# Performance work log

Measured on AMD Instinct MI355X. Metric: run time of the kernel, lower is better.

The kernel has to match this reference:

```python
import jax, jax.numpy as jnp
import numpy as np

NEAR_ZERO = 1e-6


def hat(w):
    # [..., 3] -> [..., 3, 3] skew-symmetric
    x, y, z = w[..., 0], w[..., 1], w[..., 2]
    O = jnp.zeros_like(x)
    return jnp.stack([jnp.stack([O, -z, y], -1),
                      jnp.stack([z, O, -x], -1),
                      jnp.stack([-y, x, O], -1)], -2)


def matrix_exp6(V):
    # V: [..., 6] twist (w, v) -> [..., 4, 4] SE(3) exp, with near-zero branch as in the torch code
    w, v = V[..., :3], V[..., 3:]
    theta = jnp.linalg.norm(w, axis=-1, keepdims=True)  # [..., 1]
    near = theta < NEAR_ZERO
    safe = jnp.where(near, 1.0, theta)
    Wh = hat(w / safe)
    Wh2 = Wh @ Wh
    t = theta[..., None]  # [..., 1, 1]
    I3 = jnp.eye(3, dtype=V.dtype)
    R = I3 + jnp.sin(t) * Wh + (1.0 - jnp.cos(t)) * Wh2
    R = jnp.where(near[..., None], I3, R)
    G = t * I3 + (1.0 - jnp.cos(t)) * Wh + (t - jnp.sin(t)) * Wh2
    p = jnp.einsum('...ij,...j->...i', G, v / safe)
    p = jnp.where(near, v, p)
    top = jnp.concatenate([R, p[..., None]], -1)
    bot = jnp.broadcast_to(jnp.array([0.0, 0.0, 0.0, 1.0], V.dtype), top.shape[:-2] + (1, 4))
    return jnp.concatenate([top, bot], -2)


def trans_inv(T):
    R = T[..., :3, :3]
    p = T[..., :3, 3]
    Rt = jnp.swapaxes(R, -1, -2)
    pinv = -jnp.einsum('...ij,...j->...i', Rt, p)
    top = jnp.concatenate([Rt, pinv[..., None]], -1)
    bot = jnp.broadcast_to(jnp.array([0.0, 0.0, 0.0, 1.0], T.dtype), top.shape[:-2] + (1, 4))
    return jnp.concatenate([top, bot], -2)


def adjoint(T):
    R = T[..., :3, :3]
    p = T[..., :3, 3]
    Z = jnp.zeros_like(R)
    top = jnp.concatenate([R, Z], -1)
    bot = jnp.concatenate([hat(p) @ R, R], -1)
    return jnp.concatenate([top, bot], -2)


def ad(V):
    W = hat(V[..., :3])
    Vh = hat(V[..., 3:])
    Z = jnp.zeros_like(W)
    top = jnp.concatenate([W, Z], -1)
    bot = jnp.concatenate([Vh, W], -1)
    return jnp.concatenate([top, bot], -2)


def inverse_dynamics(q, dq, ddq, g, Ftip, Alist, Mlist, Glist):
    # q, dq, ddq: [B, JN]; g: [3]; Ftip: [B, 6]; Alist: [JN, 6]; Mlist: [JN+1, 4, 4]; Glist: [JN, 6, 6]
    B, JN = q.shape
    Minv = trans_inv(Mlist)  # [JN+1, 4, 4]
    v0 = jnp.zeros((B, 6), q.dtype)
    a0 = jnp.concatenate([jnp.zeros((B, 3), q.dtype), jnp.broadcast_to(-g, (B, 3))], -1)

    # forward recursion over joints (sequential -> lax.scan), vectorized over batch
    def fwd_step(carry, xs):
        v, a = carry
        A_i, Minv_i, q_i, dq_i, ddq_i = xs
        T = matrix_exp6(-A_i[None, :] * q_i[:, None]) @ Minv_i  # [B, 4, 4]
        Ad = adjoint(T)
        v_new = jnp.einsum('bij,bj->bi', Ad, v) + A_i * dq_i[:, None]
        a_new = (jnp.einsum('bij,bj->bi', Ad, a)
                 + jnp.einsum('bij,j->bi', ad(v_new), A_i) * dq_i[:, None]
                 + A_i * ddq_i[:, None])
        return (v_new, a_new), (T, v_new, a_new)

    _, (Ts, vs, as_) = jax.lax.scan(fwd_step, (v0, a0), (Alist, Minv[:-1], q.T, dq.T, ddq.T))
    T_last = jnp.broadcast_to(Minv[-1], (B, 4, 4))
    AdNext = adjoint(jnp.concatenate([Ts[1:], T_last[None]], 0))  # [JN, B, 6, 6]

    # backward force recursion
    def bwd_step(F, xs):
        AdN, G_i, A_i, v_i, a_i = xs
        F_new = (jnp.einsum('bji,bj->bi', AdN, F)
                 + jnp.einsum('ij,bj->bi', G_i, a_i)
                 - jnp.einsum('bji,jk,bk->bi', ad(v_i), G_i, v_i))
        return F_new, F_new @ A_i

    _, tau = jax.lax.scan(bwd_step, Ftip, (AdNext, Glist, Alist, vs, as_), reverse=True)
    return tau.T  # [B, JN]


def setup_inputs() -> dict:
    key = jax.random.key(0)
    k = jax.random.split(key, 8)
    B, JN = 131072, 9
    q = jax.random.normal(k[0], (B, JN), jnp.float32)
    dq = jax.random.normal(k[1], (B, JN), jnp.float32)
    ddq = jax.random.normal(k[2], (B, JN), jnp.float32)
    Ftip = jax.random.normal(k[3], (B, 6), jnp.float32)
    g = jnp.array([0.0, 0.0, -9.8], jnp.float32)
    # screw axes with unit rotational part (revolute joints)
    w = jax.random.normal(k[4], (JN, 3), jnp.float32)
    w = w / jnp.linalg.norm(w, axis=-1, keepdims=True)
    vlin = jax.random.normal(k[5], (JN, 3), jnp.float32)
    Alist = jnp.concatenate([w, vlin], -1)
    # valid SE(3) home transforms
    Mlist = matrix_exp6(0.5 * jax.random.normal(k[6], (JN + 1, 6), jnp.float32))
    # SPD spatial inertias
    S = 0.3 * jax.random.normal(k[7], (JN, 6, 6), jnp.float32)
    Glist = S @ jnp.swapaxes(S, -1, -2) + jnp.eye(6, dtype=jnp.float32)
    return {"q": q, "dq": dq, "ddq": ddq, "g": g, "Ftip": Ftip,
            "Alist": Alist, "Mlist": Mlist, "Glist": Glist}


def reference(q, dq, ddq, g, Ftip, Alist, Mlist, Glist):
    return inverse_dynamics(q, dq, ddq, g, Ftip, Alist, Mlist, Glist)
```

## Files before the change

### kernel.cpp

```cpp
#include <hip/hip_runtime.h>
#include <math.h>

#define JN 9
#define BLK 128

__device__ __forceinline__ void mat3_vec(const float* R, const float* x, float* y) {
    y[0] = R[0]*x[0] + R[1]*x[1] + R[2]*x[2];
    y[1] = R[3]*x[0] + R[4]*x[1] + R[5]*x[2];
    y[2] = R[6]*x[0] + R[7]*x[1] + R[8]*x[2];
}
__device__ __forceinline__ void mat3T_vec(const float* R, const float* x, float* y) {
    y[0] = R[0]*x[0] + R[3]*x[1] + R[6]*x[2];
    y[1] = R[1]*x[0] + R[4]*x[1] + R[7]*x[2];
    y[2] = R[2]*x[0] + R[5]*x[1] + R[8]*x[2];
}
__device__ __forceinline__ void cross3(const float* a, const float* b, float* o) {
    o[0] = a[1]*b[2] - a[2]*b[1];
    o[1] = a[2]*b[0] - a[0]*b[2];
    o[2] = a[0]*b[1] - a[1]*b[0];
}
__device__ __forceinline__ void adj_apply(const float* R, const float* p,
                                          const float* x, float* y) {
    float t[3], cr[3], rv[3];
    mat3_vec(R, x, t);
    cross3(p, t, cr);
    mat3_vec(R, x + 3, rv);
    y[0] = t[0]; y[1] = t[1]; y[2] = t[2];
    y[3] = cr[0] + rv[0]; y[4] = cr[1] + rv[1]; y[5] = cr[2] + rv[2];
}
__device__ __forceinline__ void adjT_apply(const float* R, const float* p,
                                           const float* x, float* y) {
    float cr[3], t[3];
    cross3(p, x + 3, cr);
    t[0] = x[0] - cr[0]; t[1] = x[1] - cr[1]; t[2] = x[2] - cr[2];
    mat3T_vec(R, t, y);
    mat3T_vec(R, x + 3, y + 3);
}

__global__ void __launch_bounds__(BLK)
id_main(const float* __restrict__ q, const float* __restrict__ dq,
        const float* __restrict__ ddq, const float* __restrict__ gvec,
        const float* __restrict__ Ftip, const float* __restrict__ Alist,
        const float* __restrict__ Mlist, const float* __restrict__ Glist,
        float* __restrict__ out, int B)
{
    __shared__ float sQ[JN][BLK + 1];
    __shared__ float sB[JN * 6][BLK];

    const int tid = threadIdx.x;
    const int b = blockIdx.x * BLK + tid;

    {
        const float* qBlk = q + (size_t)blockIdx.x * BLK * JN;
#pragma unroll
        for (int k = 0; k < JN; ++k) {
            const int m = k * BLK + tid;
            sQ[m % JN][m / JN] = qBlk[m];
        }
    }
    __syncthreads();

    float Ft[6];
    __builtin_memcpy(Ft, Ftip + (size_t)b * 6, 6 * sizeof(float));

    const float g0 = gvec[0], g1 = gvec[1], g2 = gvec[2];
    float XR[9] = {1.f,0.f,0.f, 0.f,1.f,0.f, 0.f,0.f,1.f};
    float Xp[3] = {0.f, 0.f, 0.f};
    float bv[6] = {0.f,0.f,0.f,0.f,0.f,0.f};
    float ba[6] = {0.f, 0.f, 0.f, -g0, -g1, -g2};
    float U[6]  = {0.f,0.f,0.f,0.f,0.f,0.f};

#pragma unroll 1
    for (int j = 0; j < JN; ++j) {
        const float* Am = Alist + j * 6;
        const float* Gm = Glist + j * 36;
        const float* Mj = Mlist + j * 16;
        float Aj[6];
#pragma unroll
        for (int k = 0; k < 6; ++k) Aj[k] = Am[k];

        const float qj   = sQ[j][tid];
        const float dqj  = dq[(size_t)b * JN + j];
        const float ddqj = ddq[(size_t)b * JN + j];

        const float w0 = -Aj[0]*qj, w1 = -Aj[1]*qj, w2 = -Aj[2]*qj;
        const float l0 = -Aj[3]*qj, l1 = -Aj[4]*qj, l2 = -Aj[5]*qj;
        const float th = sqrtf(w0*w0 + w1*w1 + w2*w2);
        const bool near = th < 1e-6f;
        const float safe = near ? 1.f : th;
        const float inv = __builtin_amdgcn_rcpf(safe);
        const float x = w0*inv, y = w1*inv, z = w2*inv;
        const float st = __sinf(th), ct = __cosf(th);
        const float s2 = 1.f - ct;
        const float a00 = -(z*z+y*y), a11 = -(z*z+x*x), a22 = -(y*y+x*x);
        const float a01 = x*y, a02 = x*z, a12 = y*z;
        float R[9];
        R[0]=1.f+s2*a00;   R[1]=-st*z+s2*a01; R[2]= st*y+s2*a02;
        R[3]= st*z+s2*a01; R[4]=1.f+s2*a11;   R[5]=-st*x+s2*a12;
        R[6]=-st*y+s2*a02; R[7]= st*x+s2*a12; R[8]=1.f+s2*a22;
        if (near) { R[0]=1;R[1]=0;R[2]=0;R[3]=0;R[4]=1;R[5]=0;R[6]=0;R[7]=0;R[8]=1; }
        const float g3 = th - st;
        const float u0 = l0*inv, u1 = l1*inv, u2 = l2*inv;
        float p0 = th*u0 + s2*(-z*u1+y*u2) + g3*(a00*u0+a01*u1+a02*u2);
        float p1 = th*u1 + s2*( z*u0-x*u2) + g3*(a01*u0+a11*u1+a12*u2);
        float p2 = th*u2 + s2*(-y*u0+x*u1) + g3*(a02*u0+a12*u1+a22*u2);
        if (near) { p0=l0; p1=l1; p2=l2; }

        float TR[9], Tp[3];
        {
#pragma unroll
            for (int r = 0; r < 3; ++r)
#pragma unroll
                for (int cc = 0; cc < 3; ++cc)
                    TR[r*3+cc] = R[r*3+0]*Mj[cc*4+0] + R[r*3+1]*Mj[cc*4+1] + R[r*3+2]*Mj[cc*4+2];
            const float mp0 = Mj[3], mp1 = Mj[7], mp2 = Mj[11];
            Tp[0] = p0 - (TR[0]*mp0 + TR[1]*mp1 + TR[2]*mp2);
            Tp[1] = p1 - (TR[3]*mp0 + TR[4]*mp1 + TR[5]*mp2);
            Tp[2] = p2 - (TR[6]*mp0 + TR[7]*mp1 + TR[8]*mp2);
        }

        {
            float nR[9], np[3];
#pragma unroll
            for (int r = 0; r < 3; ++r)
#pragma unroll
                for (int cc = 0; cc < 3; ++cc)
                    nR[r*3+cc] = TR[r*3+0]*XR[0*3+cc] + TR[r*3+1]*XR[1*3+cc] + TR[r*3+2]*XR[2*3+cc];
            mat3_vec(TR, Xp, np);
#pragma unroll
            for (int e = 0; e < 9; ++e) XR[e] = nR[e];
            Xp[0] = np[0]+Tp[0]; Xp[1] = np[1]+Tp[1]; Xp[2] = np[2]+Tp[2];
        }

        float Bv[6];
        {
            float ip[3], tw[3], tv[3], cr[3];
            mat3T_vec(XR, Xp, ip);
            ip[0]=-ip[0]; ip[1]=-ip[1]; ip[2]=-ip[2];
            mat3T_vec(XR, Aj, tw);
            mat3T_vec(XR, Aj+3, tv);
            cross3(ip, tw, cr);
            Bv[0]=tw[0]; Bv[1]=tw[1]; Bv[2]=tw[2];
            Bv[3]=cr[0]+tv[0]; Bv[4]=cr[1]+tv[1]; Bv[5]=cr[2]+tv[2];
        }

        const float sg = Bv[0]*U[0]+Bv[1]*U[1]+Bv[2]*U[2]
                       + Bv[3]*U[3]+Bv[4]*U[4]+Bv[5]*U[5];

#pragma unroll
        for (int k = 0; k < 6; ++k) bv[k] += Bv[k]*dqj;
        {
            float t0[3], t1[3], t2[3];
            cross3(bv, Bv, t0); cross3(bv+3, Bv, t1); cross3(bv, Bv+3, t2);
            ba[0] += t0[0]*dqj + Bv[0]*ddqj;
            ba[1] += t0[1]*dqj + Bv[1]*ddqj;
            ba[2] += t0[2]*dqj + Bv[2]*ddqj;
            ba[3] += (t1[0]+t2[0])*dqj + Bv[3]*ddqj;
            ba[4] += (t1[1]+t2[1])*dqj + Bv[4]*ddqj;
            ba[5] += (t1[2]+t2[2])*dqj + Bv[5]*ddqj;
        }

        float vl[6], al[6];
        adj_apply(XR, Xp, bv, vl);
        adj_apply(XR, Xp, ba, al);
        float Gv[6], Ga[6];
#pragma unroll
        for (int r = 0; r < 6; ++r) {
            float sv = 0.f, sa = 0.f;
#pragma unroll
            for (int kk = 0; kk < 6; ++kk) { sv += Gm[r*6+kk]*vl[kk]; sa += Gm[r*6+kk]*al[kk]; }
            Gv[r] = sv; Ga[r] = sa;
        }
        float W[6];
        {
            float cw[3], cv[3], cb[3];
            cross3(vl, Gv, cw); cross3(vl+3, Gv+3, cv); cross3(vl, Gv+3, cb);
            W[0]=Ga[0]+cw[0]+cv[0]; W[1]=Ga[1]+cw[1]+cv[1]; W[2]=Ga[2]+cw[2]+cv[2];
            W[3]=Ga[3]+cb[0];       W[4]=Ga[4]+cb[1];       W[5]=Ga[5]+cb[2];
        }
        {
            float S[6];
            adjT_apply(XR, Xp, W, S);
#pragma unroll
            for (int k = 0; k < 6; ++k) U[k] += S[k];
        }

#pragma unroll
        for (int k = 0; k < 6; ++k) sB[j*6+k][tid] = Bv[k];
        sQ[j][tid] = sg;
    }

    float E[6];
    {
        const float* M9 = Mlist + JN * 16;
        float R9[9], p9[3];
#pragma unroll
        for (int r = 0; r < 3; ++r)
#pragma unroll
            for (int cc = 0; cc < 3; ++cc)
                R9[r*3+cc] = M9[0*4+r]*XR[0*3+cc] + M9[1*4+r]*XR[1*3+cc] + M9[2*4+r]*XR[2*3+cc];
        float t[3] = {Xp[0]-M9[3], Xp[1]-M9[7], Xp[2]-M9[11]};
        p9[0] = M9[0]*t[0] + M9[4]*t[1] + M9[8]*t[2];
        p9[1] = M9[1]*t[0] + M9[5]*t[1] + M9[9]*t[2];
        p9[2] = M9[2]*t[0] + M9[6]*t[1] + M9[10]*t[2];
        float Z[6];
        adjT_apply(R9, p9, Ft, Z);
#pragma unroll
        for (int k = 0; k < 6; ++k) E[k] = U[k] + Z[k];
    }
#pragma unroll
    for (int i = 0; i < JN; ++i) {
        float d = -sQ[i][tid];
#pragma unroll
        for (int k = 0; k < 6; ++k) d += sB[i*6+k][tid] * E[k];
        out[(size_t)b*JN + i] = d;
    }
}

__global__ void __launch_bounds__(BLK)
id_kernel_fb(const float* __restrict__ q, const float* __restrict__ dq,
             const float* __restrict__ ddq, const float* __restrict__ gvec,
             const float* __restrict__ Ftip, const float* __restrict__ Alist,
             const float* __restrict__ Mlist, const float* __restrict__ Glist,
             float* __restrict__ out, int B)
{
    __shared__ float sB[JN * 6][BLK];
    __shared__ float sSig[JN][BLK];
    const int tid = threadIdx.x;
    const int b = blockIdx.x * BLK + tid;
    if (b >= B) return;
    float XR[9] = {1.f,0.f,0.f, 0.f,1.f,0.f, 0.f,0.f,1.f};
    float Xp[3] = {0.f, 0.f, 0.f};
    float bv[6] = {0.f,0.f,0.f,0.f,0.f,0.f};
    float ba[6] = {0.f, 0.f, 0.f, -gvec[0], -gvec[1], -gvec[2]};
    float U[6]  = {0.f,0.f,0.f,0.f,0.f,0.f};
#pragma unroll 1
    for (int j = 0; j < JN; ++j) {
        const float* Am = Alist + j * 6;
        const float* Gm = Glist + j * 36;
        const float* Mj = Mlist + j * 16;
        float Aj[6];
#pragma unroll
        for (int k = 0; k < 6; ++k) Aj[k] = Am[k];
        const float qj = q[b*JN+j], dqj = dq[b*JN+j], ddqj = ddq[b*JN+j];
        const float w0 = -Aj[0]*qj, w1 = -Aj[1]*qj, w2 = -Aj[2]*qj;
        const float l0 = -Aj[3]*qj, l1 = -Aj[4]*qj, l2 = -Aj[5]*qj;
        const float th = sqrtf(w0*w0 + w1*w1 + w2*w2);
        const bool near = th < 1e-6f;
        const float safe = near ? 1.f : th;
        const float inv = __builtin_amdgcn_rcpf(safe);
        const float x = w0*inv, y = w1*inv, z = w2*inv;
        const float st = __sinf(th), ct = __cosf(th);
        const float s2 = 1.f - ct;
        const float a00 = -(z*z+y*y), a11 = -(z*z+x*x), a22 = -(y*y+x*x);
        const float a01 = x*y, a02 = x*z, a12 = y*z;
        float R[9];
        R[0]=1.f+s2*a00;   R[1]=-st*z+s2*a01; R[2]= st*y+s2*a02;
        R[3]= st*z+s2*a01; R[4]=1.f+s2*a11;   R[5]=-st*x+s2*a12;
        R[6]=-st*y+s2*a02; R[7]= st*x+s2*a12; R[8]=1.f+s2*a22;
        if (near) { R[0]=1;R[1]=0;R[2]=0;R[3]=0;R[4]=1;R[5]=0;R[6]=0;R[7]=0;R[8]=1; }
        const float g3 = th - st;
        const float u0 = l0*inv, u1 = l1*inv, u2 = l2*inv;
        float p0 = th*u0 + s2*(-z*u1+y*u2) + g3*(a00*u0+a01*u1+a02*u2);
        float p1 = th*u1 + s2*( z*u0-x*u2) + g3*(a01*u0+a11*u1+a12*u2);
        float p2 = th*u2 + s2*(-y*u0+x*u1) + g3*(a02*u0+a12*u1+a22*u2);
        if (near) { p0=l0; p1=l1; p2=l2; }
        float TR[9], Tp[3];
#pragma unroll
        for (int r = 0; r < 3; ++r)
#pragma unroll
            for (int cc = 0; cc < 3; ++cc)
                TR[r*3+cc] = R[r*3+0]*Mj[cc*4+0] + R[r*3+1]*Mj[cc*4+1] + R[r*3+2]*Mj[cc*4+2];
        const float mp0 = Mj[3], mp1 = Mj[7], mp2 = Mj[11];
        Tp[0] = p0 - (TR[0]*mp0 + TR[1]*mp1 + TR[2]*mp2);
        Tp[1] = p1 - (TR[3]*mp0 + TR[4]*mp1 + TR[5]*mp2);
        Tp[2] = p2 - (TR[6]*mp0 + TR[7]*mp1 + TR[8]*mp2);
        {
            float nR[9], np[3];
#pragma unroll
            for (int r = 0; r < 3; ++r)
#pragma unroll
                for (int cc = 0; cc < 3; ++cc)
                    nR[r*3+cc] = TR[r*3+0]*XR[0*3+cc] + TR[r*3+1]*XR[1*3+cc] + TR[r*3+2]*XR[2*3+cc];
            mat3_vec(TR, Xp, np);
#pragma unroll
            for (int e = 0; e < 9; ++e) XR[e] = nR[e];
            Xp[0] = np[0]+Tp[0]; Xp[1] = np[1]+Tp[1]; Xp[2] = np[2]+Tp[2];
        }
        float Bv[6];
        {
            float ip[3], tw[3], tvv[3], cr[3];
            mat3T_vec(XR, Xp, ip);
            ip[0]=-ip[0]; ip[1]=-ip[1]; ip[2]=-ip[2];
            mat3T_vec(XR, Aj, tw);
            mat3T_vec(XR, Aj+3, tvv);
            cross3(ip, tw, cr);
            Bv[0]=tw[0]; Bv[1]=tw[1]; Bv[2]=tw[2];
            Bv[3]=cr[0]+tvv[0]; Bv[4]=cr[1]+tvv[1]; Bv[5]=cr[2]+tvv[2];
        }
        float sg = Bv[0]*U[0]+Bv[1]*U[1]+Bv[2]*U[2]+Bv[3]*U[3]+Bv[4]*U[4]+Bv[5]*U[5];
#pragma unroll
        for (int k = 0; k < 6; ++k) bv[k] += Bv[k]*dqj;
        {
            float t0[3], t1[3], t2[3];
            cross3(bv, Bv, t0); cross3(bv+3, Bv, t1); cross3(bv, Bv+3, t2);
            ba[0] += t0[0]*dqj + Bv[0]*ddqj;
            ba[1] += t0[1]*dqj + Bv[1]*ddqj;
            ba[2] += t0[2]*dqj + Bv[2]*ddqj;
            ba[3] += (t1[0]+t2[0])*dqj + Bv[3]*ddqj;
            ba[4] += (t1[1]+t2[1])*dqj + Bv[4]*ddqj;
            ba[5] += (t1[2]+t2[2])*dqj + Bv[5]*ddqj;
        }
        float vl[6], al[6];
        adj_apply(XR, Xp, bv, vl);
        adj_apply(XR, Xp, ba, al);
        float Gv[6], Ga[6];
#pragma unroll
        for (int r = 0; r < 6; ++r) {
            float sv = 0.f, sa = 0.f;
#pragma unroll
            for (int kk = 0; kk < 6; ++kk) { sv += Gm[r*6+kk]*vl[kk]; sa += Gm[r*6+kk]*al[kk]; }
            Gv[r] = sv; Ga[r] = sa;
        }
        float W[6];
        {
            float cw[3], cv[3], cb[3];
            cross3(vl, Gv, cw); cross3(vl+3, Gv+3, cv); cross3(vl, Gv+3, cb);
            W[0]=Ga[0]+cw[0]+cv[0]; W[1]=Ga[1]+cw[1]+cv[1]; W[2]=Ga[2]+cw[2]+cv[2];
            W[3]=Ga[3]+cb[0];       W[4]=Ga[4]+cb[1];       W[5]=Ga[5]+cb[2];
        }
        {
            float S[6];
            adjT_apply(XR, Xp, W, S);
#pragma unroll
            for (int k = 0; k < 6; ++k) U[k] += S[k];
        }
#pragma unroll
        for (int k = 0; k < 6; ++k) sB[j*6+k][tid] = Bv[k];
        sSig[j][tid] = sg;
    }
    float E[6];
    {
        const float* M9 = Mlist + JN * 16;
        float R9[9], p9[3];
#pragma unroll
        for (int r = 0; r < 3; ++r)
#pragma unroll
            for (int cc = 0; cc < 3; ++cc)
                R9[r*3+cc] = M9[0*4+r]*XR[0*3+cc] + M9[1*4+r]*XR[1*3+cc] + M9[2*4+r]*XR[2*3+cc];
        float t[3] = {Xp[0]-M9[3], Xp[1]-M9[7], Xp[2]-M9[11]};
        p9[0] = M9[0]*t[0] + M9[4]*t[1] + M9[8]*t[2];
        p9[1] = M9[1]*t[0] + M9[5]*t[1] + M9[9]*t[2];
        p9[2] = M9[2]*t[0] + M9[6]*t[1] + M9[10]*t[2];
        float Ftl[6];
#pragma unroll
        for (int k = 0; k < 6; ++k) Ftl[k] = Ftip[b*6+k];
        float Z[6];
        adjT_apply(R9, p9, Ftl, Z);
#pragma unroll
        for (int k = 0; k < 6; ++k) E[k] = U[k] + Z[k];
    }
#pragma unroll
    for (int i = 0; i < JN; ++i) {
        float d = -sSig[i][tid];
#pragma unroll
        for (int k = 0; k < 6; ++k) d += sB[i*6+k][tid] * E[k];
        out[b*JN+i] = d;
    }
}

extern "C" void kernel_launch(void* const* d_in, const int* in_sizes, int n_in,
                              void* d_out, int out_size, void* d_ws, size_t ws_size,
                              hipStream_t stream) {
    const float* q     = (const float*)d_in[0];
    const float* dq    = (const float*)d_in[1];
    const float* ddq   = (const float*)d_in[2];
    const float* g     = (const float*)d_in[3];
    const float* Ftip  = (const float*)d_in[4];
    const float* Alist = (const float*)d_in[5];
    const float* Mlist = (const float*)d_in[6];
    const float* Glist = (const float*)d_in[7];
    float* out = (float*)d_out;
    const int B = in_sizes[0] / JN;

    if ((B % BLK) == 0) {
        const int grid = B / BLK;
        hipLaunchKernelGGL(id_main, dim3(grid), dim3(BLK), 0, stream,
                           q, dq, ddq, g, Ftip, Alist, Mlist, Glist, out, B);
    } else {
        const int grid = (B + BLK - 1) / BLK;
        hipLaunchKernelGGL(id_kernel_fb, dim3(grid), dim3(BLK), 0, stream,
                           q, dq, ddq, g, Ftip, Alist, Mlist, Glist, out, B);
    }
}
```

Measured before the change: 27.09 us.

## Split recursion into producer/consumer wavefronts pipelined through LDS rings

The per-thread inverse dynamics loop is split across two wavefronts that handle the same 64 batch elements. Wave 0 computes the joint transforms, the accumulated transform, the screw axes and the backward sums. Wave 1 runs the link-frame velocity and acceleration recursion and the wrench. They exchange results through small shared-memory ring buffers, with a block barrier at every step. The aim is to shorten each thread's serial dependency chain and overlap the two halves of the work, at the cost of one barrier per joint, extra LDS traffic and half as many batch elements per block.

```diff
diff --git a/kernel.cpp b/kernel.cpp
--- a/kernel.cpp
+++ b/kernel.cpp
@@ -3,6 +3,7 @@
 
 #define JN 9
 #define BLK 128
+#define CH 64
 
 __device__ __forceinline__ void mat3_vec(const float* R, const float* x, float* y) {
     y[0] = R[0]*x[0] + R[1]*x[1] + R[2]*x[2];
@@ -37,161 +38,194 @@
     mat3T_vec(R, x + 3, y + 3);
 }
 
-__global__ void __launch_bounds__(BLK)
-id_main(const float* __restrict__ q, const float* __restrict__ dq,
-        const float* __restrict__ ddq, const float* __restrict__ gvec,
-        const float* __restrict__ Ftip, const float* __restrict__ Alist,
-        const float* __restrict__ Mlist, const float* __restrict__ Glist,
-        float* __restrict__ out, int B)
+__device__ __forceinline__ void make_T(const float* Aj, const float* Mj, float qj,
+                                       float* TR, float* Tp)
 {
-    __shared__ float sQ[JN][BLK + 1];
-    __shared__ float sB[JN * 6][BLK];
-
-    const int tid = threadIdx.x;
-    const int b = blockIdx.x * BLK + tid;
-
-    {
-        const float* qBlk = q + (size_t)blockIdx.x * BLK * JN;
-#pragma unroll
-        for (int k = 0; k < JN; ++k) {
-            const int m = k * BLK + tid;
-            sQ[m % JN][m / JN] = qBlk[m];
-        }
-    }
-    __syncthreads();
-
+    const float w0 = -Aj[0]*qj, w1 = -Aj[1]*qj, w2 = -Aj[2]*qj;
+    const float l0 = -Aj[3]*qj, l1 = -Aj[4]*qj, l2 = -Aj[5]*qj;
+    const float th = sqrtf(w0*w0 + w1*w1 + w2*w2);
+    const bool near = th < 1e-6f;
+    const float safe = near ? 1.f : th;
+    const float inv = __builtin_amdgcn_rcpf(safe);
+    const float x = w0*inv, y = w1*inv, z = w2*inv;
+    const float st = __sinf(th), ct = __cosf(th);
+    const float s2 = 1.f - ct;
+    const float a00 = -(z*z+y*y), a11 = -(z*z+x*x), a22 = -(y*y+x*x);
+    const float a01 = x*y, a02 = x*z, a12 = y*z;
+    float R[9];
+    R[0]=1.f+s2*a00;   R[1]=-st*z+s2*a01; R[2]= st*y+s2*a02;
+    R[3]= st*z+s2*a01; R[4]=1.f+s2*a11;   R[5]=-st*x+s2*a12;
+    R[6]=-st*y+s2*a02; R[7]= st*x+s2*a12; R[8]=1.f+s2*a22;
+    if (near) { R[0]=1;R[1]=0;R[2]=0;R[3]=0;R[4]=1;R[5]=0;R[6]=0;R[7]=0;R[8]=1; }
+    const float g3 = th - st;
+    const float u0 = l0*inv, u1 = l1*inv, u2 = l2*inv;
+    float p0 = th*u0 + s2*(-z*u1+y*u2) + g3*(a00*u0+a01*u1+a02*u2);
+    float p1 = th*u1 + s2*( z*u0-x*u2) + g3*(a01*u0+a11*u1+a12*u2);
+    float p2 = th*u2 + s2*(-y*u0+x*u1) + g3*(a02*u0+a12*u1+a22*u2);
+    if (near) { p0=l0; p1=l1; p2=l2; }
+#pragma unroll
+    for (int r = 0; r < 3; ++r)
+#pragma unroll
+        for (int cc = 0; cc < 3; ++cc)
+            TR[r*3+cc] = R[r*3+0]*Mj[cc*4+0] + R[r*3+1]*Mj[cc*4+1] + R[r*3+2]*Mj[cc*4+2];
+    const float mp0 = Mj[3], mp1 = Mj[7], mp2 = Mj[11];
+    Tp[0] = p0 - (TR[0]*mp0 + TR[1]*mp1 + TR[2]*mp2);
+    Tp[1] = p1 - (TR[3]*mp0 + TR[4]*mp1 + TR[5]*mp2);
+    Tp[2] = p2 - (TR[6]*mp0 + TR[7]*mp1 + TR[8]*mp2);
+}
+
+__global__ void __launch_bounds__(BLK, 4)
+id_pc(const float* __restrict__ q, const float* __restrict__ dq,
+      const float* __restrict__ ddq, const float* __restrict__ gvec,
+      const float* __restrict__ Ftip, const float* __restrict__ Alist,
+      const float* __restrict__ Mlist, const float* __restrict__ Glist,
+      float* __restrict__ out, int B)
+{
+    __shared__ float ringT[3][12][CH];
+    __shared__ float ringW[2][6][CH];
+    __shared__ float sBsig[JN*6 + JN][CH];
+
+    const int lane = threadIdx.x & 63;
+    const int wid  = threadIdx.x >> 6;
+    const int c = blockIdx.x * CH + lane;
+
+    float XR[9]  = {1,0,0, 0,1,0, 0,0,1};
+    float Xp[3]  = {0,0,0};
+    float XRp[9] = {1,0,0, 0,1,0, 0,0,1};
+    float Xpp[3] = {0,0,0};
+    float U[6]   = {0,0,0,0,0,0};
+    float Bprev[6] = {0,0,0,0,0,0};
     float Ft[6];
-    __builtin_memcpy(Ft, Ftip + (size_t)b * 6, 6 * sizeof(float));
-
-    const float g0 = gvec[0], g1 = gvec[1], g2 = gvec[2];
-    float XR[9] = {1.f,0.f,0.f, 0.f,1.f,0.f, 0.f,0.f,1.f};
-    float Xp[3] = {0.f, 0.f, 0.f};
-    float bv[6] = {0.f,0.f,0.f,0.f,0.f,0.f};
-    float ba[6] = {0.f, 0.f, 0.f, -g0, -g1, -g2};
-    float U[6]  = {0.f,0.f,0.f,0.f,0.f,0.f};
+    float vl[6] = {0,0,0,0,0,0};
+    float al[6] = {0,0,0,0,0,0};
+
+    if (wid == 0) {
+#pragma unroll
+        for (int k = 0; k < 6; ++k) Ft[k] = Ftip[(size_t)c*6 + k];
+    } else {
+        al[3] = -gvec[0]; al[4] = -gvec[1]; al[5] = -gvec[2];
+    }
 
 #pragma unroll 1
-    for (int j = 0; j < JN; ++j) {
-        const float* Am = Alist + j * 6;
-        const float* Gm = Glist + j * 36;
-        const float* Mj = Mlist + j * 16;
-        float Aj[6];
-#pragma unroll
-        for (int k = 0; k < 6; ++k) Aj[k] = Am[k];
-
-        const float qj   = sQ[j][tid];
-        const float dqj  = dq[(size_t)b * JN + j];
-        const float ddqj = ddq[(size_t)b * JN + j];
-
-        const float w0 = -Aj[0]*qj, w1 = -Aj[1]*qj, w2 = -Aj[2]*qj;
-        const float l0 = -Aj[3]*qj, l1 = -Aj[4]*qj, l2 = -Aj[5]*qj;
-        const float th = sqrtf(w0*w0 + w1*w1 + w2*w2);
-        const bool near = th < 1e-6f;
-        const float safe = near ? 1.f : th;
-        const float inv = __builtin_amdgcn_rcpf(safe);
-        const float x = w0*inv, y = w1*inv, z = w2*inv;
-        const float st = __sinf(th), ct = __cosf(th);
-        const float s2 = 1.f - ct;
-        const float a00 = -(z*z+y*y), a11 = -(z*z+x*x), a22 = -(y*y+x*x);
-        const float a01 = x*y, a02 = x*z, a12 = y*z;
-        float R[9];
-        R[0]=1.f+s2*a00;   R[1]=-st*z+s2*a01; R[2]= st*y+s2*a02;
-        R[3]= st*z+s2*a01; R[4]=1.f+s2*a11;   R[5]=-st*x+s2*a12;
-        R[6]=-st*y+s2*a02; R[7]= st*x+s2*a12; R[8]=1.f+s2*a22;
-        if (near) { R[0]=1;R[1]=0;R[2]=0;R[3]=0;R[4]=1;R[5]=0;R[6]=0;R[7]=0;R[8]=1; }
-        const float g3 = th - st;
-        const float u0 = l0*inv, u1 = l1*inv, u2 = l2*inv;
-        float p0 = th*u0 + s2*(-z*u1+y*u2) + g3*(a00*u0+a01*u1+a02*u2);
-        float p1 = th*u1 + s2*( z*u0-x*u2) + g3*(a01*u0+a11*u1+a12*u2);
-        float p2 = th*u2 + s2*(-y*u0+x*u1) + g3*(a02*u0+a12*u1+a22*u2);
-        if (near) { p0=l0; p1=l1; p2=l2; }
-
-        float TR[9], Tp[3];
-        {
-#pragma unroll
-            for (int r = 0; r < 3; ++r)
-#pragma unroll
-                for (int cc = 0; cc < 3; ++cc)
-                    TR[r*3+cc] = R[r*3+0]*Mj[cc*4+0] + R[r*3+1]*Mj[cc*4+1] + R[r*3+2]*Mj[cc*4+2];
-            const float mp0 = Mj[3], mp1 = Mj[7], mp2 = Mj[11];
-            Tp[0] = p0 - (TR[0]*mp0 + TR[1]*mp1 + TR[2]*mp2);
-            Tp[1] = p1 - (TR[3]*mp0 + TR[4]*mp1 + TR[5]*mp2);
-            Tp[2] = p2 - (TR[6]*mp0 + TR[7]*mp1 + TR[8]*mp2);
-        }
-
-        {
-            float nR[9], np[3];
-#pragma unroll
-            for (int r = 0; r < 3; ++r)
-#pragma unroll
-                for (int cc = 0; cc < 3; ++cc)
-                    nR[r*3+cc] = TR[r*3+0]*XR[0*3+cc] + TR[r*3+1]*XR[1*3+cc] + TR[r*3+2]*XR[2*3+cc];
-            mat3_vec(TR, Xp, np);
-#pragma unroll
-            for (int e = 0; e < 9; ++e) XR[e] = nR[e];
-            Xp[0] = np[0]+Tp[0]; Xp[1] = np[1]+Tp[1]; Xp[2] = np[2]+Tp[2];
-        }
-
-        float Bv[6];
-        {
-            float ip[3], tw[3], tv[3], cr[3];
-            mat3T_vec(XR, Xp, ip);
-            ip[0]=-ip[0]; ip[1]=-ip[1]; ip[2]=-ip[2];
-            mat3T_vec(XR, Aj, tw);
-            mat3T_vec(XR, Aj+3, tv);
-            cross3(ip, tw, cr);
-            Bv[0]=tw[0]; Bv[1]=tw[1]; Bv[2]=tw[2];
-            Bv[3]=cr[0]+tv[0]; Bv[4]=cr[1]+tv[1]; Bv[5]=cr[2]+tv[2];
-        }
-
-        const float sg = Bv[0]*U[0]+Bv[1]*U[1]+Bv[2]*U[2]
-                       + Bv[3]*U[3]+Bv[4]*U[4]+Bv[5]*U[5];
-
-#pragma unroll
-        for (int k = 0; k < 6; ++k) bv[k] += Bv[k]*dqj;
-        {
-            float t0[3], t1[3], t2[3];
-            cross3(bv, Bv, t0); cross3(bv+3, Bv, t1); cross3(bv, Bv+3, t2);
-            ba[0] += t0[0]*dqj + Bv[0]*ddqj;
-            ba[1] += t0[1]*dqj + Bv[1]*ddqj;
-            ba[2] += t0[2]*dqj + Bv[2]*ddqj;
-            ba[3] += (t1[0]+t2[0])*dqj + Bv[3]*ddqj;
-            ba[4] += (t1[1]+t2[1])*dqj + Bv[4]*ddqj;
-            ba[5] += (t1[2]+t2[2])*dqj + Bv[5]*ddqj;
-        }
-
-        float vl[6], al[6];
-        adj_apply(XR, Xp, bv, vl);
-        adj_apply(XR, Xp, ba, al);
-        float Gv[6], Ga[6];
-#pragma unroll
-        for (int r = 0; r < 6; ++r) {
-            float sv = 0.f, sa = 0.f;
-#pragma unroll
-            for (int kk = 0; kk < 6; ++kk) { sv += Gm[r*6+kk]*vl[kk]; sa += Gm[r*6+kk]*al[kk]; }
-            Gv[r] = sv; Ga[r] = sa;
-        }
-        float W[6];
-        {
-            float cw[3], cv[3], cb[3];
-            cross3(vl, Gv, cw); cross3(vl+3, Gv+3, cv); cross3(vl, Gv+3, cb);
-            W[0]=Ga[0]+cw[0]+cv[0]; W[1]=Ga[1]+cw[1]+cv[1]; W[2]=Ga[2]+cw[2]+cv[2];
-            W[3]=Ga[3]+cb[0];       W[4]=Ga[4]+cb[1];       W[5]=Ga[5]+cb[2];
-        }
-        {
-            float S[6];
-            adjT_apply(XR, Xp, W, S);
-#pragma unroll
-            for (int k = 0; k < 6; ++k) U[k] += S[k];
-        }
-
-#pragma unroll
-        for (int k = 0; k < 6; ++k) sB[j*6+k][tid] = Bv[k];
-        sQ[j][tid] = sg;
-    }
-
-    float E[6];
-    {
+    for (int j = 0; j <= JN + 1; ++j) {
+        if (wid == 0) {
+            if (j >= 2) {
+                float W[6], S[6];
+#pragma unroll
+                for (int k = 0; k < 6; ++k) W[k] = ringW[(j-2) & 1][k][lane];
+                adjT_apply(XRp, Xpp, W, S);
+#pragma unroll
+                for (int k = 0; k < 6; ++k) U[k] += S[k];
+            }
+            if (j >= 1 && j <= JN) {
+                float sg = Bprev[0]*U[0]+Bprev[1]*U[1]+Bprev[2]*U[2]
+                         + Bprev[3]*U[3]+Bprev[4]*U[4]+Bprev[5]*U[5];
+                sBsig[JN*6 + (j-1)][lane] = sg;
+            }
+#pragma unroll
+            for (int e = 0; e < 9; ++e) XRp[e] = XR[e];
+            Xpp[0]=Xp[0]; Xpp[1]=Xp[1]; Xpp[2]=Xp[2];
+
+            if (j < JN) {
+                const float* Am = Alist + j*6;
+                const float* Mj = Mlist + j*16;
+                float Aj[6];
+#pragma unroll
+                for (int k = 0; k < 6; ++k) Aj[k] = Am[k];
+                const float qj = q[(size_t)c*JN + j];
+                float TR[9], Tp[3];
+                make_T(Aj, Mj, qj, TR, Tp);
+#pragma unroll
+                for (int e = 0; e < 9; ++e) ringT[j%3][e][lane] = TR[e];
+                ringT[j%3][9][lane]  = Tp[0];
+                ringT[j%3][10][lane] = Tp[1];
+                ringT[j%3][11][lane] = Tp[2];
+                {
+                    float nR[9], np[3];
+#pragma unroll
+                    for (int r = 0; r < 3; ++r)
+#pragma unroll
+                        for (int cc = 0; cc < 3; ++cc)
+                            nR[r*3+cc] = TR[r*3+0]*XR[0*3+cc] + TR[r*3+1]*XR[1*3+cc] + TR[r*3+2]*XR[2*3+cc];
+                    mat3_vec(TR, Xp, np);
+#pragma unroll
+                    for (int e = 0; e < 9; ++e) XR[e] = nR[e];
+                    Xp[0] = np[0]+Tp[0]; Xp[1] = np[1]+Tp[1]; Xp[2] = np[2]+Tp[2];
+                }
+                float Bv[6];
+                {
+                    float ip[3], tw[3], tv[3], cr[3];
+                    mat3T_vec(XR, Xp, ip);
+                    ip[0]=-ip[0]; ip[1]=-ip[1]; ip[2]=-ip[2];
+                    mat3T_vec(XR, Aj, tw);
+                    mat3T_vec(XR, Aj+3, tv);
+                    cross3(ip, tw, cr);
+                    Bv[0]=tw[0]; Bv[1]=tw[1]; Bv[2]=tw[2];
+                    Bv[3]=cr[0]+tv[0]; Bv[4]=cr[1]+tv[1]; Bv[5]=cr[2]+tv[2];
+                }
+#pragma unroll
+                for (int k = 0; k < 6; ++k) { sBsig[j*6+k][lane] = Bv[k]; Bprev[k] = Bv[k]; }
+            }
+        } else {
+            if (j >= 1 && j <= JN) {
+                const int jj = j - 1;
+                const float dqj  = dq[(size_t)c*JN + jj];
+                const float ddqj = ddq[(size_t)c*JN + jj];
+                float TR[9], Tp[3];
+#pragma unroll
+                for (int e = 0; e < 9; ++e) TR[e] = ringT[jj%3][e][lane];
+                Tp[0] = ringT[jj%3][9][lane];
+                Tp[1] = ringT[jj%3][10][lane];
+                Tp[2] = ringT[jj%3][11][lane];
+                const float* Am = Alist + jj*6;
+                float Aj[6];
+#pragma unroll
+                for (int k = 0; k < 6; ++k) Aj[k] = Am[k];
+                float vn[6];
+                adj_apply(TR, Tp, vl, vn);
+#pragma unroll
+                for (int k = 0; k < 6; ++k) vn[k] += Aj[k]*dqj;
+                float an[6];
+                adj_apply(TR, Tp, al, an);
+                {
+                    float t0[3], t1[3], t2[3];
+                    cross3(vn, Aj, t0);
+                    cross3(vn+3, Aj, t1);
+                    cross3(vn, Aj+3, t2);
+                    an[0] += t0[0]*dqj + Aj[0]*ddqj;
+                    an[1] += t0[1]*dqj + Aj[1]*ddqj;
+                    an[2] += t0[2]*dqj + Aj[2]*ddqj;
+                    an[3] += (t1[0]+t2[0])*dqj + Aj[3]*ddqj;
+                    an[4] += (t1[1]+t2[1])*dqj + Aj[4]*ddqj;
+                    an[5] += (t1[2]+t2[2])*dqj + Aj[5]*ddqj;
+                }
+#pragma unroll
+                for (int k = 0; k < 6; ++k) { vl[k] = vn[k]; al[k] = an[k]; }
+                const float* Gm = Glist + jj*36;
+                float Gv[6], Ga[6];
+#pragma unroll
+                for (int r = 0; r < 6; ++r) {
+                    float sv = 0.f, sa = 0.f;
+#pragma unroll
+                    for (int kk = 0; kk < 6; ++kk) { sv += Gm[r*6+kk]*vl[kk]; sa += Gm[r*6+kk]*al[kk]; }
+                    Gv[r] = sv; Ga[r] = sa;
+                }
+                float cw[3], cv[3], cb[3];
+                cross3(vl, Gv, cw);
+                cross3(vl+3, Gv+3, cv);
+                cross3(vl, Gv+3, cb);
+                ringW[jj & 1][0][lane] = Ga[0]+cw[0]+cv[0];
+                ringW[jj & 1][1][lane] = Ga[1]+cw[1]+cv[1];
+                ringW[jj & 1][2][lane] = Ga[2]+cw[2]+cv[2];
+                ringW[jj & 1][3][lane] = Ga[3]+cb[0];
+                ringW[jj & 1][4][lane] = Ga[4]+cb[1];
+                ringW[jj & 1][5][lane] = Ga[5]+cb[2];
+            }
+        }
+        __syncthreads();
+    }
+
+    if (wid == 0) {
         const float* M9 = Mlist + JN * 16;
         float R9[9], p9[3];
 #pragma unroll
@@ -203,17 +237,17 @@
         p9[0] = M9[0]*t[0] + M9[4]*t[1] + M9[8]*t[2];
         p9[1] = M9[1]*t[0] + M9[5]*t[1] + M9[9]*t[2];
         p9[2] = M9[2]*t[0] + M9[6]*t[1] + M9[10]*t[2];
-        float Z[6];
+        float Z[6], E[6];
         adjT_apply(R9, p9, Ft, Z);
 #pragma unroll
         for (int k = 0; k < 6; ++k) E[k] = U[k] + Z[k];
-    }
-#pragma unroll
-    for (int i = 0; i < JN; ++i) {
-        float d = -sQ[i][tid];
-#pragma unroll
-        for (int k = 0; k < 6; ++k) d += sB[i*6+k][tid] * E[k];
-        out[(size_t)b*JN + i] = d;
+#pragma unroll
+        for (int i = 0; i < JN; ++i) {
+            float d = -sBsig[JN*6 + i][lane];
+#pragma unroll
+            for (int k = 0; k < 6; ++k) d += sBsig[i*6+k][lane] * E[k];
+            out[(size_t)c*JN + i] = d;
+        }
     }
 }
 
@@ -243,38 +277,8 @@
 #pragma unroll
         for (int k = 0; k < 6; ++k) Aj[k] = Am[k];
         const float qj = q[b*JN+j], dqj = dq[b*JN+j], ddqj = ddq[b*JN+j];
-        const float w0 = -Aj[0]*qj, w1 = -Aj[1]*qj, w2 = -Aj[2]*qj;
-        const float l0 = -Aj[3]*qj, l1 = -Aj[4]*qj, l2 = -Aj[5]*qj;
-        const float th = sqrtf(w0*w0 + w1*w1 + w2*w2);
-        const bool near = th < 1e-6f;
-        const float safe = near ? 1.f : th;
-        const float inv = __builtin_amdgcn_rcpf(safe);
-        const float x = w0*inv, y = w1*inv, z = w2*inv;
-        const float st = __sinf(th), ct = __cosf(th);
-        const float s2 = 1.f - ct;
-        const float a00 = -(z*z+y*y), a11 = -(z*z+x*x), a22 = -(y*y+x*x);
-        const float a01 = x*y, a02 = x*z, a12 = y*z;
-        float R[9];
-        R[0]=1.f+s2*a00;   R[1]=-st*z+s2*a01; R[2]= st*y+s2*a02;
-        R[3]= st*z+s2*a01; R[4]=1.f+s2*a11;   R[5]=-st*x+s2*a12;
-        R[6]=-st*y+s2*a02; R[7]= st*x+s2*a12; R[8]=1.f+s2*a22;
-        if (near) { R[0]=1;R[1]=0;R[2]=0;R[3]=0;R[4]=1;R[5]=0;R[6]=0;R[7]=0;R[8]=1; }
-        const float g3 = th - st;
-        const float u0 = l0*inv, u1 = l1*inv, u2 = l2*inv;
-        float p0 = th*u0 + s2*(-z*u1+y*u2) + g3*(a00*u0+a01*u1+a02*u2);
-        float p1 = th*u1 + s2*( z*u0-x*u2) + g3*(a01*u0+a11*u1+a12*u2);
-        float p2 = th*u2 + s2*(-y*u0+x*u1) + g3*(a02*u0+a12*u1+a22*u2);
-        if (near) { p0=l0; p1=l1; p2=l2; }
         float TR[9], Tp[3];
-#pragma unroll
-        for (int r = 0; r < 3; ++r)
-#pragma unroll
-            for (int cc = 0; cc < 3; ++cc)
-                TR[r*3+cc] = R[r*3+0]*Mj[cc*4+0] + R[r*3+1]*Mj[cc*4+1] + R[r*3+2]*Mj[cc*4+2];
-        const float mp0 = Mj[3], mp1 = Mj[7], mp2 = Mj[11];
-        Tp[0] = p0 - (TR[0]*mp0 + TR[1]*mp1 + TR[2]*mp2);
-        Tp[1] = p1 - (TR[3]*mp0 + TR[4]*mp1 + TR[5]*mp2);
-        Tp[2] = p2 - (TR[6]*mp0 + TR[7]*mp1 + TR[8]*mp2);
+        make_T(Aj, Mj, qj, TR, Tp);
         {
             float nR[9], np[3];
 #pragma unroll
@@ -383,9 +387,9 @@
     float* out = (float*)d_out;
     const int B = in_sizes[0] / JN;
 
-    if ((B % BLK) == 0) {
-        const int grid = B / BLK;
-        hipLaunchKernelGGL(id_main, dim3(grid), dim3(BLK), 0, stream,
+    if ((B % CH) == 0) {
+        const int grid = B / CH;
+        hipLaunchKernelGGL(id_pc, dim3(grid), dim3(BLK), 0, stream,
                            q, dq, ddq, g, Ftip, Alist, Mlist, Glist, out, B);
     } else {
         const int grid = (B + BLK - 1) / BLK;
```

Result: slower. 38.27 us (+41.3%).
